# Kernel optimization log

Measured on AMD Instinct MI355X. Metric: run time of the kernel, lower is better.

Reference implementation:

```python
import jax, jax.numpy as jnp
import numpy as np

B, T, D, H = 2, 2048, 1024, 16
HD = D // H  # head_dim = 64


def apply_rope(x, cos, sin):
    # x: [B, H, T, HD]; cos/sin: [1, 1, T, HD//2]
    x1, x2 = x[..., ::2], x[..., 1::2]
    y1 = x1 * cos - x2 * sin
    y2 = x1 * sin + x2 * cos
    # interleave back: [..., HD//2, 2] -> [..., HD]
    return jnp.stack([y1, y2], axis=-1).reshape(x.shape)


def setup_inputs() -> dict:
    key = jax.random.key(0)
    ks = jax.random.split(key, 11)
    s = 0.02
    return {
        "x": jax.random.normal(ks[0], (B, T, D), jnp.float32),
        "cos": jax.random.normal(ks[1], (1, 1, T, HD // 2), jnp.float32),
        "sin": jax.random.normal(ks[2], (1, 1, T, HD // 2), jnp.float32),
        "Wq": jax.random.normal(ks[3], (D, D), jnp.float32) * s,
        "bq": jax.random.normal(ks[4], (D,), jnp.float32) * s,
        "Wk": jax.random.normal(ks[5], (D, D), jnp.float32) * s,
        "bk": jax.random.normal(ks[6], (D,), jnp.float32) * s,
        "Wv": jax.random.normal(ks[7], (D, D), jnp.float32) * s,
        "bv": jax.random.normal(ks[8], (D,), jnp.float32) * s,
        "Wo": jax.random.normal(ks[9], (D, D), jnp.float32) * s,
        "bo": jax.random.normal(ks[10], (D,), jnp.float32) * s,
    }


def reference(x, cos, sin, Wq, bq, Wk, bk, Wv, bv, Wo, bo):
    b, t, d = x.shape
    # projections (nn.Linear: x @ W.T + b)
    q = (x @ Wq.T + bq).reshape(b, t, H, HD).transpose(0, 2, 1, 3)
    k = (x @ Wk.T + bk).reshape(b, t, H, HD).transpose(0, 2, 1, 3)
    v = (x @ Wv.T + bv).reshape(b, t, H, HD).transpose(0, 2, 1, 3)
    q = apply_rope(q, cos, sin)
    k = apply_rope(k, cos, sin)
    scores = jnp.einsum("bhqd,bhkd->bhqk", q, k) / jnp.sqrt(jnp.asarray(HD, x.dtype))
    # causal mask: query i attends to keys j <= i
    causal = jnp.tril(jnp.ones((t, t), dtype=bool))
    scores = jnp.where(causal, scores, jnp.asarray(-jnp.inf, x.dtype))
    weights = jax.nn.softmax(scores, axis=-1)
    out = jnp.einsum("bhqk,bhkd->bhqd", weights, v)
    out = out.transpose(0, 2, 1, 3).reshape(b, t, d)
    return out @ Wo.T + bo
```

## Files before the change

kernel.cpp:

```cpp
#include <hip/hip_runtime.h>
#include <hip/hip_bf16.h>
#include <cstdint>
#include <cstddef>

typedef __attribute__((ext_vector_type(8))) short bf16x8;
typedef __attribute__((ext_vector_type(4))) float f32x4;
typedef __attribute__((ext_vector_type(16))) float f32x16;

#define SCALE2 0.180336880111112f
#define VSTRIDE 2080

__device__ __forceinline__ unsigned short f2bf(float f) {
    unsigned u = __builtin_bit_cast(unsigned, f);
    unsigned r = (u + 0x7FFFu + ((u >> 16) & 1u)) >> 16;
    return (unsigned short)r;
}

__device__ __forceinline__ void gload16(const unsigned short* g, unsigned short* l) {
    __builtin_amdgcn_global_load_lds(
        (const __attribute__((address_space(1))) unsigned int*)(g),
        (__attribute__((address_space(3))) unsigned int*)(l), 16, 0, 0);
}

__global__ void cvt_all(const float* __restrict__ x,
                        const float* __restrict__ wq, const float* __restrict__ wk,
                        const float* __restrict__ wv, const float* __restrict__ wo,
                        unsigned short* __restrict__ xb,
                        unsigned short* __restrict__ wqb, unsigned short* __restrict__ wkb,
                        unsigned short* __restrict__ wvb, unsigned short* __restrict__ wob)
{
    const int y = blockIdx.y;
    const float* src; unsigned short* dst; int n;
    switch (y) {
        case 0: src = x;  dst = xb;  n = 4194304; break;
        case 1: src = wq; dst = wqb; n = 1048576; break;
        case 2: src = wk; dst = wkb; n = 1048576; break;
        case 3: src = wv; dst = wvb; n = 1048576; break;
        default: src = wo; dst = wob; n = 1048576; break;
    }
    const int i = (blockIdx.x * 256 + threadIdx.x) * 4;
    if (i < n) {
        float4 v = *(const float4*)(src + i);
        ushort4 o;
        o.x = f2bf(v.x); o.y = f2bf(v.y); o.z = f2bf(v.z); o.w = f2bf(v.w);
        *(ushort4*)(dst + i) = o;
    }
}

__global__ __launch_bounds__(256) void gemm_qkv(
    const unsigned short* __restrict__ xb,
    const unsigned short* __restrict__ wqb,
    const unsigned short* __restrict__ wkb,
    const unsigned short* __restrict__ wvb,
    const float* __restrict__ bq, const float* __restrict__ bk, const float* __restrict__ bv,
    const float* __restrict__ cosT, const float* __restrict__ sinT,
    unsigned short* __restrict__ Qb, unsigned short* __restrict__ Kb, unsigned short* __restrict__ Vtg)
{
    const int bid = blockIdx.x;
    const int xcd = bid & 7;
    const int s = bid >> 3;
    const int i4 = xcd >> 1, k2 = xcd & 1;
    const int z = s >> 5;
    const int tt = s & 31;
    const int m0 = (i4 * 8 + (tt >> 2)) * 128;
    const int n0 = (k2 * 4 + (tt & 3)) * 128;

    const unsigned short* wb = (z == 0) ? wqb : ((z == 1) ? wkb : wvb);
    const float* bias = (z == 0) ? bq : ((z == 1) ? bk : bv);
    unsigned short* dst = (z == 0) ? Qb : Kb;

    __shared__ __align__(16) unsigned short Al[128 * 32];
    __shared__ __align__(16) unsigned short Bl[128 * 32];
    __shared__ __align__(16) unsigned short Ct[128 * 136];

    const int tid = threadIdx.x;
    const int lane = tid & 63;
    const int w = tid >> 6;
    const int wr = w >> 1, wc = w & 1;
    const int lr = lane & 15, lg = lane >> 4;
    const int srow = tid >> 2, sseg = tid & 3;
    const int wbase = tid & 192;

    f32x4 acc[4][4] = {};

    for (int k0 = 0; k0 < 1024; k0 += 32) {
        __syncthreads();
#pragma unroll
        for (int p = 0; p < 2; ++p) {
            const int row = srow + p * 64;
            gload16(xb + (size_t)(m0 + row) * 1024 + k0 + sseg * 8, Al + (p * 256 + wbase) * 8);
            gload16(wb + (size_t)(n0 + row) * 1024 + k0 + sseg * 8, Bl + (p * 256 + wbase) * 8);
        }
        __syncthreads();
        bf16x8 af[4], bfr[4];
#pragma unroll
        for (int mt = 0; mt < 4; ++mt)
            af[mt] = *(const bf16x8*)(Al + (wr * 64 + mt * 16 + lr) * 32 + lg * 8);
#pragma unroll
        for (int nt = 0; nt < 4; ++nt)
            bfr[nt] = *(const bf16x8*)(Bl + (wc * 64 + nt * 16 + lr) * 32 + lg * 8);
#pragma unroll
        for (int mt = 0; mt < 4; ++mt)
#pragma unroll
            for (int nt = 0; nt < 4; ++nt)
                acc[mt][nt] = __builtin_amdgcn_mfma_f32_16x16x32_bf16(af[mt], bfr[nt], acc[mt][nt], 0, 0, 0);
    }

#pragma unroll
    for (int mt = 0; mt < 4; ++mt) {
#pragma unroll
        for (int nt = 0; nt < 4; ++nt) {
            const int coln = wc * 64 + nt * 16 + lr;
            const int col = n0 + coln;
            const float bcol = bias[col];
            const int hd = col & 63;
#pragma unroll
            for (int r = 0; r < 4; ++r) {
                const int rowm = wr * 64 + mt * 16 + lg * 4 + r;
                float v = acc[mt][nt][r] + bcol;
                if (z < 2) {
                    float part = __shfl_xor(v, 1);
                    const int ttm = (m0 + rowm) & 2047;
                    const int i = hd >> 1;
                    const float cc = cosT[ttm * 32 + i], ss = sinT[ttm * 32 + i];
                    v = (hd & 1) ? (part * ss + v * cc) : (v * cc - part * ss);
                    if (z == 0) v *= SCALE2;
                    Ct[rowm * 136 + coln] = f2bf(v);
                } else {
                    Ct[coln * 136 + rowm] = f2bf(v);
                }
            }
        }
    }
    __syncthreads();
    if (z < 2) {
#pragma unroll
        for (int p = 0; p < 8; ++p) {
            const int u = p * 256 + tid;
            const int row = u >> 4, seg = u & 15;
            bf16x8 vv = *(const bf16x8*)(Ct + row * 136 + seg * 8);
            const int mrow = m0 + row;
            const int ttm = mrow & 2047, bb = mrow >> 11;
            const int col = n0 + seg * 8;
            const int h = col >> 6, hd = col & 63;
            *(bf16x8*)(dst + ((size_t)(bb * 16 + h) * 2048 + ttm) * 64 + hd) = vv;
        }
    } else {
        const int bb = m0 >> 11;
#pragma unroll
        for (int p = 0; p < 8; ++p) {
            const int u = p * 256 + tid;
            const int vrow = u >> 4, seg = u & 15;
            bf16x8 vv = *(const bf16x8*)(Ct + vrow * 136 + seg * 8);
            const int col = n0 + vrow;
            const int h = col >> 6, hd = col & 63;
            const int ttm = (m0 + seg * 8) & 2047;
            *(bf16x8*)(Vtg + ((size_t)(bb * 16 + h) * 64 + hd) * VSTRIDE + ttm) = vv;
        }
    }
}

__global__ __launch_bounds__(256, 2) void attn_fwd(
    const unsigned short* __restrict__ Qb, const unsigned short* __restrict__ Kb,
    const unsigned short* __restrict__ Vtg, unsigned short* __restrict__ attnb)
{
    __shared__ __align__(16) unsigned char smem[25088];

    const int tid = threadIdx.x, lane = tid & 63, w = tid >> 6;
    const int l31 = lane & 31, lh = lane >> 5;
    const int bid = blockIdx.x;
    const int bh = bid & 31;
    const int pi = bid >> 5;
    const int half = w >> 1;
    const int slice = w & 1;
    const int cH = 63 - pi;
    const int c = half ? pi : cH;
    const size_t base = (size_t)bh * 131072;
    const int myq = c * 32 + l31;

    const unsigned short* Kg = Kb + base;
    const unsigned short* Vg = Vtg + (size_t)bh * (64 * VSTRIDE);

    bf16x8 qf[4];
#pragma unroll
    for (int s = 0; s < 4; ++s)
        qf[s] = *(const bf16x8*)(Qb + base + (size_t)myq * 64 + s * 16 + lh * 8);

    f32x16 o0 = {}, o1 = {};
    float sm = 0.f;

    const int krow = tid >> 3, kseg = (tid & 7) ^ (krow & 7);
    const int vrow = tid >> 2, vseg = (tid & 3) ^ (vrow & 3);
    const int ldst = (tid & ~63) * 8;

#define STAGE(T, B)                                                                   \
    {                                                                                 \
        unsigned short* kb_ = (unsigned short*)(smem + (B) * 8192);                   \
        unsigned short* vb_ = (unsigned short*)(smem + (B) * 8192 + 4096);            \
        gload16(Kg + (size_t)((T) * 32 + krow) * 64 + kseg * 8, kb_ + ldst);          \
        gload16(Vg + (size_t)vrow * VSTRIDE + (T) * 32 + vseg * 8, vb_ + ldst);       \
    }

    STAGE(0, 0);
    STAGE(1, 1);
    int bsel = 0;
    for (int t = 0; t <= cH; ++t) {
        if (t < cH) asm volatile("s_waitcnt vmcnt(2)" ::: "memory");
        else        asm volatile("s_waitcnt vmcnt(0)" ::: "memory");
        __syncthreads();
        {
            const int t2 = t + 2;
            if (t2 <= cH) {
                int b2 = bsel + 2; if (b2 >= 3) b2 -= 3;
                STAGE(t2, b2);
            }
        }
        if (t <= c && (t & 1) == slice) {
            const unsigned short* Kc = (const unsigned short*)(smem + bsel * 8192);
            const unsigned short* Vc = Kc + 2048;
            const int kvb = t * 32;

            bf16x8 kf0 = *(const bf16x8*)(Kc + l31 * 64 + ((0 * 2 + lh) ^ (l31 & 7)) * 8);
            bf16x8 kf1 = *(const bf16x8*)(Kc + l31 * 64 + ((1 * 2 + lh) ^ (l31 & 7)) * 8);
            bf16x8 kf2 = *(const bf16x8*)(Kc + l31 * 64 + ((2 * 2 + lh) ^ (l31 & 7)) * 8);
            bf16x8 kf3 = *(const bf16x8*)(Kc + l31 * 64 + ((3 * 2 + lh) ^ (l31 & 7)) * 8);

            f32x16 st = {};
            st = __builtin_amdgcn_mfma_f32_32x32x16_bf16(kf0, qf[0], st, 0, 0, 0);
            st = __builtin_amdgcn_mfma_f32_32x32x16_bf16(kf1, qf[1], st, 0, 0, 0);
            st = __builtin_amdgcn_mfma_f32_32x32x16_bf16(kf2, qf[2], st, 0, 0, 0);
            st = __builtin_amdgcn_mfma_f32_32x32x16_bf16(kf3, qf[3], st, 0, 0, 0);

            if (t == c) {
#pragma unroll
                for (int r = 0; r < 16; ++r) {
                    const int kv = kvb + (r & 3) + 8 * (r >> 2) + 4 * lh;
                    st[r] = (kv <= myq) ? st[r] : -1e30f;
                }
            }
#pragma unroll
            for (int r = 0; r < 16; ++r) st[r] = exp2f(st[r]);
            {
                float a0 = st[0] + st[1], a1 = st[2] + st[3];
                float a2 = st[4] + st[5], a3 = st[6] + st[7];
                float a4 = st[8] + st[9], a5 = st[10] + st[11];
                float a6 = st[12] + st[13], a7 = st[14] + st[15];
                sm += ((a0 + a1) + (a2 + a3)) + ((a4 + a5) + (a6 + a7));
            }

            unsigned pw0, pw1, pw2, pw3, pw4, pw5, pw6, pw7;
            {
                unsigned a0, a1, b0, b1;
                asm("v_cvt_pk_bf16_f32 %0, %1, %2" : "=v"(a0) : "v"(st[0]), "v"(st[1]));
                asm("v_cvt_pk_bf16_f32 %0, %1, %2" : "=v"(a1) : "v"(st[2]), "v"(st[3]));
                asm("v_cvt_pk_bf16_f32 %0, %1, %2" : "=v"(b0) : "v"(st[4]), "v"(st[5]));
                asm("v_cvt_pk_bf16_f32 %0, %1, %2" : "=v"(b1) : "v"(st[6]), "v"(st[7]));
                asm("v_permlane32_swap_b32 %0, %1" : "+v"(a0), "+v"(b0));
                asm("v_permlane32_swap_b32 %0, %1" : "+v"(a1), "+v"(b1));
                pw0 = a0; pw1 = a1; pw2 = b0; pw3 = b1;
            }
            {
                unsigned a0, a1, b0, b1;
                asm("v_cvt_pk_bf16_f32 %0, %1, %2" : "=v"(a0) : "v"(st[8]), "v"(st[9]));
                asm("v_cvt_pk_bf16_f32 %0, %1, %2" : "=v"(a1) : "v"(st[10]), "v"(st[11]));
                asm("v_cvt_pk_bf16_f32 %0, %1, %2" : "=v"(b0) : "v"(st[12]), "v"(st[13]));
                asm("v_cvt_pk_bf16_f32 %0, %1, %2" : "=v"(b1) : "v"(st[14]), "v"(st[15]));
                asm("v_permlane32_swap_b32 %0, %1" : "+v"(a0), "+v"(b0));
                asm("v_permlane32_swap_b32 %0, %1" : "+v"(a1), "+v"(b1));
                pw4 = a0; pw5 = a1; pw6 = b0; pw7 = b1;
            }

            const int vsw = l31 & 3;
            bf16x8 vf00 = *(const bf16x8*)(Vc + l31 * 32 + ((lh) ^ vsw) * 8);
            bf16x8 vf01 = *(const bf16x8*)(Vc + l31 * 32 + ((2 + lh) ^ vsw) * 8);
            bf16x8 vf10 = *(const bf16x8*)(Vc + (32 + l31) * 32 + ((lh) ^ vsw) * 8);
            bf16x8 vf11 = *(const bf16x8*)(Vc + (32 + l31) * 32 + ((2 + lh) ^ vsw) * 8);

            uint4 h0 = make_uint4(pw0, pw1, pw2, pw3);
            uint4 h1 = make_uint4(pw4, pw5, pw6, pw7);
            bf16x8 pf0 = __builtin_bit_cast(bf16x8, h0);
            bf16x8 pf1 = __builtin_bit_cast(bf16x8, h1);
            o0 = __builtin_amdgcn_mfma_f32_32x32x16_bf16(vf00, pf0, o0, 0, 0, 0);
            o1 = __builtin_amdgcn_mfma_f32_32x32x16_bf16(vf10, pf0, o1, 0, 0, 0);
            o0 = __builtin_amdgcn_mfma_f32_32x32x16_bf16(vf01, pf1, o0, 0, 0, 0);
            o1 = __builtin_amdgcn_mfma_f32_32x32x16_bf16(vf11, pf1, o1, 0, 0, 0);
        }
        bsel += 1; if (bsel == 3) bsel = 0;
    }

    sm += __shfl_xor(sm, 32);

    float* Om = (float*)smem;
    float* Ms = (float*)(smem + 16384);
    __syncthreads();
    if (slice == 1) {
#pragma unroll
        for (int i = 0; i < 16; ++i) Om[(half * 32 + i) * 64 + lane] = o0[i];
#pragma unroll
        for (int i = 0; i < 16; ++i) Om[(half * 32 + 16 + i) * 64 + lane] = o1[i];
        Ms[half * 64 + lane] = sm;
    }
    __syncthreads();
    if (slice == 0) {
        const float s = sm + Ms[half * 64 + lane];
        const float inv = 1.f / s;
        const int b = bh >> 4, h = bh & 15;
        unsigned short* obase = attnb + ((size_t)(b * 2048 + myq)) * 1024 + h * 64;
#pragma unroll
        for (int g = 0; g < 4; ++g) {
            ushort4 u;
            u.x = f2bf((o0[g * 4 + 0] + Om[(half * 32 + g * 4 + 0) * 64 + lane]) * inv);
            u.y = f2bf((o0[g * 4 + 1] + Om[(half * 32 + g * 4 + 1) * 64 + lane]) * inv);
            u.z = f2bf((o0[g * 4 + 2] + Om[(half * 32 + g * 4 + 2) * 64 + lane]) * inv);
            u.w = f2bf((o0[g * 4 + 3] + Om[(half * 32 + g * 4 + 3) * 64 + lane]) * inv);
            *(ushort4*)(obase + g * 8 + lh * 4) = u;
            ushort4 v;
            v.x = f2bf((o1[g * 4 + 0] + Om[(half * 32 + 16 + g * 4 + 0) * 64 + lane]) * inv);
            v.y = f2bf((o1[g * 4 + 1] + Om[(half * 32 + 16 + g * 4 + 1) * 64 + lane]) * inv);
            v.z = f2bf((o1[g * 4 + 2] + Om[(half * 32 + 16 + g * 4 + 2) * 64 + lane]) * inv);
            v.w = f2bf((o1[g * 4 + 3] + Om[(half * 32 + 16 + g * 4 + 3) * 64 + lane]) * inv);
            *(ushort4*)(obase + 32 + g * 8 + lh * 4) = v;
        }
    }
#undef STAGE
}

__global__ __launch_bounds__(256) void gemm_out(
    const unsigned short* __restrict__ ab,
    const unsigned short* __restrict__ wob,
    const float* __restrict__ bo,
    float* __restrict__ out)
{
    __shared__ __align__(16) unsigned short Al[128 * 32];
    __shared__ __align__(16) unsigned short Bl[64 * 32];

    const int bid = blockIdx.x;
    const int xcd = bid & 7;
    const int s = bid >> 3;
    const int i4 = xcd >> 1, k2 = xcd & 1;
    const int m0 = (i4 * 8 + (s >> 3)) * 128;
    const int n0 = (k2 * 8 + (s & 7)) * 64;

    const int tid = threadIdx.x;
    const int lane = tid & 63;
    const int w = tid >> 6;
    const int lr = lane & 15, lg = lane >> 4;

    f32x4 acc[2][4] = {};

    for (int k0 = 0; k0 < 1024; k0 += 32) {
        __syncthreads();
#pragma unroll
        for (int p = 0; p < 2; ++p) {
            const int u = p * 256 + tid;
            const int row = u >> 2, seg = u & 3;
            gload16(ab + (size_t)(m0 + row) * 1024 + k0 + seg * 8, Al + (u & ~63) * 8);
        }
        {
            const int u = tid;
            const int row = u >> 2, seg = u & 3;
            gload16(wob + (size_t)(n0 + row) * 1024 + k0 + seg * 8, Bl + (u & ~63) * 8);
        }
        __syncthreads();
        bf16x8 af[2], bfr[4];
#pragma unroll
        for (int mt = 0; mt < 2; ++mt)
            af[mt] = *(const bf16x8*)(Al + (w * 32 + mt * 16 + lr) * 32 + lg * 8);
#pragma unroll
        for (int nt = 0; nt < 4; ++nt)
            bfr[nt] = *(const bf16x8*)(Bl + (nt * 16 + lr) * 32 + lg * 8);
#pragma unroll
        for (int mt = 0; mt < 2; ++mt)
#pragma unroll
            for (int nt = 0; nt < 4; ++nt)
                acc[mt][nt] = __builtin_amdgcn_mfma_f32_16x16x32_bf16(af[mt], bfr[nt], acc[mt][nt], 0, 0, 0);
    }

#pragma unroll
    for (int mt = 0; mt < 2; ++mt) {
#pragma unroll
        for (int nt = 0; nt < 4; ++nt) {
            const int col = n0 + nt * 16 + lr;
            const float bcol = bo[col];
#pragma unroll
            for (int r = 0; r < 4; ++r) {
                const int mrow = m0 + w * 32 + mt * 16 + lg * 4 + r;
                out[(size_t)mrow * 1024 + col] = acc[mt][nt][r] + bcol;
            }
        }
    }
}

extern "C" void kernel_launch(void* const* d_in, const int* in_sizes, int n_in,
                              void* d_out, int out_size, void* d_ws, size_t ws_size,
                              hipStream_t stream) {
    const float* x    = (const float*)d_in[0];
    const float* cosT = (const float*)d_in[1];
    const float* sinT = (const float*)d_in[2];
    const float* Wq   = (const float*)d_in[3];
    const float* bq   = (const float*)d_in[4];
    const float* Wk   = (const float*)d_in[5];
    const float* bk   = (const float*)d_in[6];
    const float* Wv   = (const float*)d_in[7];
    const float* bv   = (const float*)d_in[8];
    const float* Wo   = (const float*)d_in[9];
    const float* bo   = (const float*)d_in[10];
    float* out = (float*)d_out;

    char* ws = (char*)d_ws;
    unsigned short* xb    = (unsigned short*)(ws + 0);
    unsigned short* attnb = (unsigned short*)(ws + 0);
    unsigned short* wob   = (unsigned short*)(ws + 8388608);
    unsigned short* wqb   = (unsigned short*)(ws + 10485760);
    unsigned short* wkb   = (unsigned short*)(ws + 12582912);
    unsigned short* wvb   = (unsigned short*)(ws + 14680064);
    unsigned short* Qb    = (unsigned short*)(ws + 16777216);
    unsigned short* Kb    = (unsigned short*)(ws + 25165824);
    unsigned short* Vtg   = (unsigned short*)(ws + 33554432);

    cvt_all<<<dim3(4096, 5), 256, 0, stream>>>(x, Wq, Wk, Wv, Wo, xb, wqb, wkb, wvb, wob);
    gemm_qkv<<<dim3(768), 256, 0, stream>>>(xb, wqb, wkb, wvb, bq, bk, bv,
                                            cosT, sinT, Qb, Kb, Vtg);
    attn_fwd<<<dim3(1024), 256, 0, stream>>>(Qb, Kb, Vtg, attnb);
    gemm_out<<<dim3(512), 256, 0, stream>>>(attnb, wob, bo, out);
}
```

Before: 119.1 us.

## Split attention KV loop across four waves per query tile, one tile per block

Before, each block paired two causal query tiles (a short and a long one) for load balance, and each half split the KV tiles between two waves. Now each block handles a single 32-query tile, and all four waves take KV tiles round-robin, so the grid doubles to 2048 blocks. Partial outputs are reduced through shared memory at the end. The V shared-memory swizzle is also changed to a different XOR pattern to cut bank conflicts. This trades the explicit causal load balancing for more blocks and a larger cross-wave reduction, and blocks for early query tiles now do very little work.

```diff
diff --git a/kernel.cpp b/kernel.cpp
--- a/kernel.cpp
+++ b/kernel.cpp
@@ -164,17 +164,13 @@
     const unsigned short* __restrict__ Qb, const unsigned short* __restrict__ Kb,
     const unsigned short* __restrict__ Vtg, unsigned short* __restrict__ attnb)
 {
-    __shared__ __align__(16) unsigned char smem[25088];
+    __shared__ __align__(16) unsigned char smem[25344];
 
     const int tid = threadIdx.x, lane = tid & 63, w = tid >> 6;
     const int l31 = lane & 31, lh = lane >> 5;
     const int bid = blockIdx.x;
     const int bh = bid & 31;
-    const int pi = bid >> 5;
-    const int half = w >> 1;
-    const int slice = w & 1;
-    const int cH = 63 - pi;
-    const int c = half ? pi : cH;
+    const int c = 63 - (bid >> 5);
     const size_t base = (size_t)bh * 131072;
     const int myq = c * 32 + l31;
 
@@ -190,7 +186,7 @@
     float sm = 0.f;
 
     const int krow = tid >> 3, kseg = (tid & 7) ^ (krow & 7);
-    const int vrow = tid >> 2, vseg = (tid & 3) ^ (vrow & 3);
+    const int vrow = tid >> 2, vseg = (tid & 3) ^ ((vrow >> 1) & 3);
     const int ldst = (tid & ~63) * 8;
 
 #define STAGE(T, B)                                                                   \
@@ -202,20 +198,17 @@
     }
 
     STAGE(0, 0);
-    STAGE(1, 1);
+    if (c >= 1) STAGE(1, 1);
     int bsel = 0;
-    for (int t = 0; t <= cH; ++t) {
-        if (t < cH) asm volatile("s_waitcnt vmcnt(2)" ::: "memory");
-        else        asm volatile("s_waitcnt vmcnt(0)" ::: "memory");
+    for (int t = 0; t <= c; ++t) {
+        if (t < c) asm volatile("s_waitcnt vmcnt(2)" ::: "memory");
+        else       asm volatile("s_waitcnt vmcnt(0)" ::: "memory");
         __syncthreads();
-        {
-            const int t2 = t + 2;
-            if (t2 <= cH) {
-                int b2 = bsel + 2; if (b2 >= 3) b2 -= 3;
-                STAGE(t2, b2);
-            }
-        }
-        if (t <= c && (t & 1) == slice) {
+        if (t + 2 <= c) {
+            int b2 = bsel + 2; if (b2 >= 3) b2 -= 3;
+            STAGE(t + 2, b2);
+        }
+        if ((t & 3) == w) {
             const unsigned short* Kc = (const unsigned short*)(smem + bsel * 8192);
             const unsigned short* Vc = Kc + 2048;
             const int kvb = t * 32;
@@ -270,11 +263,11 @@
                 pw4 = a0; pw5 = a1; pw6 = b0; pw7 = b1;
             }
 
-            const int vsw = l31 & 3;
-            bf16x8 vf00 = *(const bf16x8*)(Vc + l31 * 32 + ((lh) ^ vsw) * 8);
-            bf16x8 vf01 = *(const bf16x8*)(Vc + l31 * 32 + ((2 + lh) ^ vsw) * 8);
-            bf16x8 vf10 = *(const bf16x8*)(Vc + (32 + l31) * 32 + ((lh) ^ vsw) * 8);
-            bf16x8 vf11 = *(const bf16x8*)(Vc + (32 + l31) * 32 + ((2 + lh) ^ vsw) * 8);
+            const int g0 = (l31 >> 1) & 3;
+            bf16x8 vf00 = *(const bf16x8*)(Vc + l31 * 32 + ((lh ^ g0)) * 8);
+            bf16x8 vf01 = *(const bf16x8*)(Vc + l31 * 32 + (((2 + lh) ^ g0)) * 8);
+            bf16x8 vf10 = *(const bf16x8*)(Vc + (32 + l31) * 32 + ((lh ^ g0)) * 8);
+            bf16x8 vf11 = *(const bf16x8*)(Vc + (32 + l31) * 32 + (((2 + lh) ^ g0)) * 8);
 
             uint4 h0 = make_uint4(pw0, pw1, pw2, pw3);
             uint4 h1 = make_uint4(pw4, pw5, pw6, pw7);
@@ -291,34 +284,42 @@
     sm += __shfl_xor(sm, 32);
 
     float* Om = (float*)smem;
-    float* Ms = (float*)(smem + 16384);
+    float* Ms = (float*)(smem + 24576);
     __syncthreads();
-    if (slice == 1) {
-#pragma unroll
-        for (int i = 0; i < 16; ++i) Om[(half * 32 + i) * 64 + lane] = o0[i];
-#pragma unroll
-        for (int i = 0; i < 16; ++i) Om[(half * 32 + 16 + i) * 64 + lane] = o1[i];
-        Ms[half * 64 + lane] = sm;
+    if (w > 0) {
+#pragma unroll
+        for (int i = 0; i < 16; ++i) Om[((w - 1) * 32 + i) * 64 + lane] = o0[i];
+#pragma unroll
+        for (int i = 0; i < 16; ++i) Om[((w - 1) * 32 + 16 + i) * 64 + lane] = o1[i];
+        Ms[(w - 1) * 64 + lane] = sm;
     }
     __syncthreads();
-    if (slice == 0) {
-        const float s = sm + Ms[half * 64 + lane];
+    if (w == 0) {
+        const float s = sm + Ms[0 * 64 + lane] + Ms[1 * 64 + lane] + Ms[2 * 64 + lane];
         const float inv = 1.f / s;
         const int b = bh >> 4, h = bh & 15;
         unsigned short* obase = attnb + ((size_t)(b * 2048 + myq)) * 1024 + h * 64;
 #pragma unroll
         for (int g = 0; g < 4; ++g) {
             ushort4 u;
-            u.x = f2bf((o0[g * 4 + 0] + Om[(half * 32 + g * 4 + 0) * 64 + lane]) * inv);
-            u.y = f2bf((o0[g * 4 + 1] + Om[(half * 32 + g * 4 + 1) * 64 + lane]) * inv);
-            u.z = f2bf((o0[g * 4 + 2] + Om[(half * 32 + g * 4 + 2) * 64 + lane]) * inv);
-            u.w = f2bf((o0[g * 4 + 3] + Om[(half * 32 + g * 4 + 3) * 64 + lane]) * inv);
+#pragma unroll
+            for (int j = 0; j < 4; ++j) {
+                const int i = g * 4 + j;
+                float acc = o0[i] + Om[(0 * 32 + i) * 64 + lane]
+                                  + Om[(1 * 32 + i) * 64 + lane]
+                                  + Om[(2 * 32 + i) * 64 + lane];
+                ((unsigned short*)&u)[j] = f2bf(acc * inv);
+            }
             *(ushort4*)(obase + g * 8 + lh * 4) = u;
             ushort4 v;
-            v.x = f2bf((o1[g * 4 + 0] + Om[(half * 32 + 16 + g * 4 + 0) * 64 + lane]) * inv);
-            v.y = f2bf((o1[g * 4 + 1] + Om[(half * 32 + 16 + g * 4 + 1) * 64 + lane]) * inv);
-            v.z = f2bf((o1[g * 4 + 2] + Om[(half * 32 + 16 + g * 4 + 2) * 64 + lane]) * inv);
-            v.w = f2bf((o1[g * 4 + 3] + Om[(half * 32 + 16 + g * 4 + 3) * 64 + lane]) * inv);
+#pragma unroll
+            for (int j = 0; j < 4; ++j) {
+                const int i = g * 4 + j;
+                float acc = o1[i] + Om[(0 * 32 + 16 + i) * 64 + lane]
+                                  + Om[(1 * 32 + 16 + i) * 64 + lane]
+                                  + Om[(2 * 32 + 16 + i) * 64 + lane];
+                ((unsigned short*)&v)[j] = f2bf(acc * inv);
+            }
             *(ushort4*)(obase + 32 + g * 8 + lh * 4) = v;
         }
     }
@@ -421,6 +422,6 @@
     cvt_all<<<dim3(4096, 5), 256, 0, stream>>>(x, Wq, Wk, Wv, Wo, xb, wqb, wkb, wvb, wob);
     gemm_qkv<<<dim3(768), 256, 0, stream>>>(xb, wqb, wkb, wvb, bq, bk, bv,
                                             cosT, sinT, Qb, Kb, Vtg);
-    attn_fwd<<<dim3(1024), 256, 0, stream>>>(Qb, Kb, Vtg, attnb);
+    attn_fwd<<<dim3(2048), 256, 0, stream>>>(Qb, Kb, Vtg, attnb);
     gemm_out<<<dim3(512), 256, 0, stream>>>(attnb, wob, bo, out);
 }
```

New measurement: 126.8 us. 6.4% more time.
